# Optimization experiments

Measured on AMD Instinct MI355X. Metric: run time of the kernel, lower is better.

## Reference

```python
import jax, jax.numpy as jnp
import numpy as np

DIM = 1024
N_HEAD = 16
HEAD_DIM = DIM // N_HEAD


def setup_inputs() -> dict:
    key = jax.random.key(0)
    ks = jax.random.split(key, 5)
    scale = 0.02
    x = jax.random.normal(ks[0], (4, 2048, DIM), dtype=jnp.float32)
    W_qkv = jax.random.normal(ks[1], (DIM, 3 * DIM), dtype=jnp.float32) * scale
    b_qkv = jnp.zeros((3 * DIM,), dtype=jnp.float32)
    W_proj = jax.random.normal(ks[2], (DIM, DIM), dtype=jnp.float32) * scale
    b_proj = jnp.zeros((DIM,), dtype=jnp.float32)
    return {"x": x, "W_qkv": W_qkv, "b_qkv": b_qkv, "W_proj": W_proj, "b_proj": b_proj}


def reference(x, W_qkv, b_qkv, W_proj, b_proj):
    B, N, C = x.shape
    qkv = x @ W_qkv + b_qkv                       # [B,N,3C]
    qkv = qkv.reshape(B, N, 3, N_HEAD, HEAD_DIM)
    q, k, v = qkv[:, :, 0], qkv[:, :, 1], qkv[:, :, 2]   # [B,N,H,d]
    # scores: [B,H,N,N]
    att = jnp.einsum('bnhd,bmhd->bhnm', q, k) * (1.0 / np.sqrt(HEAD_DIM))
    att = jax.nn.softmax(att, axis=-1)
    out = jnp.einsum('bhnm,bmhd->bnhd', att, v).reshape(B, N, C)
    return out @ W_proj + b_proj
```

## Files before the change

### kernel.cpp

```cpp
#include <hip/hip_runtime.h>
#include <stdint.h>

#define DEV __device__ __forceinline__

typedef __bf16 bf16x8 __attribute__((ext_vector_type(8)));
typedef float f32x2 __attribute__((ext_vector_type(2)));
typedef float f32x4 __attribute__((ext_vector_type(4)));
typedef float f32x16 __attribute__((ext_vector_type(16)));

DEV uint16_t f2bf(float f) {
  union { float f; uint32_t u; } v; v.f = f;
  return (uint16_t)((v.u + 0x7FFFu + ((v.u >> 16) & 1u)) >> 16);
}

DEV f32x2 pkadd(f32x2 a, f32x2 b) {
  f32x2 d;
  asm("v_pk_add_f32 %0, %1, %2" : "=v"(d) : "v"(a), "v"(b));
  return d;
}

#define GLD_LDS(gsrc, ldst)                                                   \
  __builtin_amdgcn_global_load_lds(                                           \
      (__attribute__((address_space(1))) void*)(void*)(gsrc),                 \
      (__attribute__((address_space(3))) void*)(ldst), 16, 0, 0)

__global__ __launch_bounds__(256) void k_prep(const float* __restrict__ x,
                                              const float* __restrict__ Wqkv,
                                              const float* __restrict__ Wproj,
                                              uint16_t* __restrict__ xb,
                                              uint16_t* __restrict__ wqkvt,
                                              uint16_t* __restrict__ wprojt) {
  __shared__ float tile[32][33];
  int bid = blockIdx.x;
  if (bid < 4096) {
    int i = bid * 256 + threadIdx.x;
    const float4* p = (const float4*)x;
    float4 a = p[i * 2], b = p[i * 2 + 1];
    union { uint16_t s[8]; uint4 v; } o;
    o.s[0] = f2bf(a.x); o.s[1] = f2bf(a.y); o.s[2] = f2bf(a.z); o.s[3] = f2bf(a.w);
    o.s[4] = f2bf(b.x); o.s[5] = f2bf(b.y); o.s[6] = f2bf(b.z); o.s[7] = f2bf(b.w);
    ((uint4*)xb)[i] = o.v;
    return;
  }
  const float* in;
  uint16_t* out;
  int n0, k0, Ncols;
  if (bid < 7168) {
    int local = bid - 4096;
    in = Wqkv; out = wqkvt; Ncols = 3072;
    n0 = (local % 96) * 32; k0 = (local / 96) * 32;
  } else {
    int local = bid - 7168;
    in = Wproj; out = wprojt; Ncols = 1024;
    n0 = (local % 32) * 32; k0 = (local / 32) * 32;
  }
  int tx = threadIdx.x & 31, ty = threadIdx.x >> 5;
  #pragma unroll
  for (int r = ty; r < 32; r += 8)
    tile[r][tx] = in[(size_t)(k0 + r) * Ncols + n0 + tx];
  __syncthreads();
  #pragma unroll
  for (int r = ty; r < 32; r += 8)
    out[(size_t)(n0 + r) * 1024 + k0 + tx] = f2bf(tile[tx][r]);
}

template <int MODE>
__global__ __launch_bounds__(256) void k_gemm(
    const uint16_t* __restrict__ A, const uint16_t* __restrict__ BT,
    const float* __restrict__ bias, float* __restrict__ fout, int Ndim,
    uint16_t* __restrict__ qb, uint16_t* __restrict__ kb,
    uint16_t* __restrict__ vtb) {
  __shared__ uint16_t As[2][128 * 32];
  __shared__ uint16_t Bs[2][128 * 32];
  const int K = 1024;
  int tid = threadIdx.x;
  int lane = tid & 63, wid = tid >> 6;
  int lg = lane >> 4, lr = lane & 15;
  int wr = wid >> 1, wc = wid & 1;
  int bm = blockIdx.x, bn = blockIdx.y;

  int c0 = tid, c1 = tid + 256;
  int r0 = c0 >> 2, sl0 = (c0 & 3) ^ (r0 & 3);
  int r1 = c1 >> 2, sl1 = (c1 & 3) ^ (r1 & 3);
  const uint16_t* gA0 = A + (size_t)(bm * 128 + r0) * K + sl0 * 8;
  const uint16_t* gA1 = A + (size_t)(bm * 128 + r1) * K + sl1 * 8;
  const uint16_t* gB0 = BT + (size_t)(bn * 128 + r0) * K + sl0 * 8;
  const uint16_t* gB1 = BT + (size_t)(bn * 128 + r1) * K + sl1 * 8;

  uint32_t aoff[4], boff[4];
  #pragma unroll
  for (int i = 0; i < 4; ++i) {
    int rowa = wr * 64 + i * 16 + lr;
    aoff[i] = rowa * 64 + ((lg ^ (rowa & 3)) << 4);
    int rowb = wc * 64 + i * 16 + lr;
    boff[i] = rowb * 64 + ((lg ^ (rowb & 3)) << 4);
  }

  f32x4 acc[4][4] = {};

  auto stageg = [&](int buf) {
    GLD_LDS(gA0, &As[buf][wid * 512]);
    GLD_LDS(gA1, &As[buf][2048 + wid * 512]);
    GLD_LDS(gB0, &Bs[buf][wid * 512]);
    GLD_LDS(gB1, &Bs[buf][2048 + wid * 512]);
    gA0 += 32; gA1 += 32; gB0 += 32; gB1 += 32;
  };

  auto gbody = [&](int cur, bool dostage) {
    if (dostage) stageg(cur ^ 1);
    const char* Ab = (const char*)As + cur * 8192;
    const char* Bb = (const char*)Bs + cur * 8192;
    bf16x8 af[4], bfv[4];
    #pragma unroll
    for (int i = 0; i < 4; ++i) af[i] = *(const bf16x8*)(Ab + aoff[i]);
    #pragma unroll
    for (int j = 0; j < 4; ++j) bfv[j] = *(const bf16x8*)(Bb + boff[j]);
    __builtin_amdgcn_s_setprio(1);
    #pragma unroll
    for (int i = 0; i < 4; ++i)
      #pragma unroll
      for (int j = 0; j < 4; ++j)
        acc[i][j] = __builtin_amdgcn_mfma_f32_16x16x32_bf16(af[i], bfv[j],
                                                            acc[i][j], 0, 0, 0);
    __builtin_amdgcn_s_setprio(0);
    __syncthreads();
  };

  stageg(0);
  __syncthreads();
  for (int ks = 0; ks < 30; ks += 2) {
    gbody(0, true);
    gbody(1, true);
  }
  gbody(0, true);
  gbody(1, false);

  int m0 = bm * 128 + wr * 64;
  int n0 = bn * 128 + wc * 64;
  if (MODE == 1) {
    #pragma unroll
    for (int i = 0; i < 4; ++i) {
      int row = m0 + i * 16 + lg * 4;
      #pragma unroll
      for (int j = 0; j < 4; ++j) {
        int col = n0 + j * 16 + lr;
        float bv = bias[col];
        #pragma unroll
        for (int r = 0; r < 4; ++r)
          fout[(size_t)(row + r) * Ndim + col] = acc[i][j][r] + bv;
      }
    }
  } else {
    const float QSC = 0.18033688011112042f;
    #pragma unroll
    for (int i = 0; i < 4; ++i) {
      int rowb = m0 + i * 16 + lg * 4;
      int b = rowb >> 11, t = rowb & 2047;
      #pragma unroll
      for (int j = 0; j < 4; ++j) {
        int colb = n0 + j * 16 + lr;
        int which = colb >> 10;
        int hd = colb & 1023;
        int h = hd >> 6, d = hd & 63;
        float bv = bias[colb];
        size_t bh = (size_t)(b * 16 + h);
        if (which == 2) {
          union { uint16_t s[4]; uint2 v; } pk;
          #pragma unroll
          for (int r = 0; r < 4; ++r) pk.s[r] = f2bf(acc[i][j][r] + bv);
          *(uint2*)&vtb[(bh * 64 + d) * 2048 + t] = pk.v;
        } else {
          uint16_t* dst = which ? kb : qb;
          float sc = which ? 1.f : QSC;
          #pragma unroll
          for (int r = 0; r < 4; ++r)
            dst[(bh * 2048 + t + r) * 64 + d] = f2bf((acc[i][j][r] + bv) * sc);
        }
      }
    }
  }
}

__global__ __launch_bounds__(256) void k_attn(const uint16_t* __restrict__ qb,
                                              const uint16_t* __restrict__ kb,
                                              const uint16_t* __restrict__ vtb,
                                              uint16_t* __restrict__ ob) {
  __shared__ uint16_t SM[4][64 * 64];
  int tid = threadIdx.x, lane = tid & 63, wid = tid >> 6;
  int l31 = lane & 31, hi = lane >> 5;
  int rx = (l31 & 7) ^ (((l31 >> 3) & 3) << 1);
  int bid = blockIdx.x;
  int bh = (bid & 7) * 8 + ((bid >> 3) & 7);
  int qt = bid >> 6;
  const uint16_t* qbh = qb + (size_t)bh * 2048 * 64;
  const uint16_t* kbh = kb + (size_t)bh * 2048 * 64;
  const uint16_t* vbh = vtb + (size_t)bh * 64 * 2048;
  int q = qt * 128 + wid * 32 + l31;

  uint32_t koff[8];
  #pragma unroll
  for (int kvt = 0; kvt < 2; ++kvt)
    #pragma unroll
    for (int ks = 0; ks < 4; ++ks)
      koff[kvt * 4 + ks] = (kvt * 32 + l31) * 128 + (((ks * 2 + hi) ^ rx) << 4);

  bf16x8 qf[4];
  #pragma unroll
  for (int ks = 0; ks < 4; ++ks)
    qf[ks] = *(const bf16x8*)(qbh + (size_t)q * 64 + ks * 16 + hi * 8);

  f32x16 ovt[2] = {};
  f32x2 lr2 = {0.f, 0.f};

  int r0 = tid >> 3;
  int sx = (tid & 7) ^ (r0 & 7) ^ (((r0 >> 3) & 3) << 1);
  const uint16_t* kp0 = kbh + (size_t)r0 * 64 + sx * 8;
  const uint16_t* kp1 = kbh + (size_t)(r0 + 32) * 64 + sx * 8;
  const uint16_t* vp0 = vbh + (size_t)r0 * 2048 + sx * 8;
  const uint16_t* vp1 = vbh + (size_t)(r0 + 32) * 2048 + sx * 8;

  auto stage = [&](int buf) {
    uint16_t* KN = &SM[buf][0];
    uint16_t* VN = &SM[2 + buf][0];
    GLD_LDS(kp0, KN + wid * 512);
    GLD_LDS(kp1, KN + 2048 + wid * 512);
    GLD_LDS(vp0, VN + wid * 512);
    GLD_LDS(vp1, VN + 2048 + wid * 512);
    kp0 += 4096; kp1 += 4096; vp0 += 64; vp1 += 64;
  };

  auto body = [&](int cur, bool dostage) {
    if (dostage) stage(cur ^ 1);
    const char* Kc = (const char*)SM + cur * 8192;
    const char* Vc = (const char*)SM + 16384 + cur * 8192;

    f32x16 sv[2] = {};
    __builtin_amdgcn_s_setprio(1);
    #pragma unroll
    for (int kvt = 0; kvt < 2; ++kvt)
      #pragma unroll
      for (int ks = 0; ks < 4; ++ks) {
        bf16x8 kf = *(const bf16x8*)(Kc + koff[kvt * 4 + ks]);
        sv[kvt] = __builtin_amdgcn_mfma_f32_32x32x16_bf16(kf, qf[ks], sv[kvt], 0, 0, 0);
      }
    __builtin_amdgcn_s_setprio(0);

    #pragma unroll
    for (int t = 0; t < 2; ++t)
      #pragma unroll
      for (int r = 0; r < 16; ++r) sv[t][r] = __builtin_amdgcn_exp2f(sv[t][r]);

    #define SVP(t, i) __builtin_shufflevector(sv[t], sv[t], 2 * (i), 2 * (i) + 1)
    f32x2 s0 = pkadd(pkadd(pkadd(SVP(0, 0), SVP(0, 1)), pkadd(SVP(0, 2), SVP(0, 3))),
                     pkadd(pkadd(SVP(0, 4), SVP(0, 5)), pkadd(SVP(0, 6), SVP(0, 7))));
    f32x2 s1 = pkadd(pkadd(pkadd(SVP(1, 0), SVP(1, 1)), pkadd(SVP(1, 2), SVP(1, 3))),
                     pkadd(pkadd(SVP(1, 4), SVP(1, 5)), pkadd(SVP(1, 6), SVP(1, 7))));
    #undef SVP
    lr2 = pkadd(lr2, pkadd(s0, s1));

    union PB { uint32_t w[4]; bf16x8 v; } pb[4];
    #pragma unroll
    for (int t = 0; t < 2; ++t)
      #pragma unroll
      for (int s = 0; s < 2; ++s) {
        int rb = s * 8;
        #pragma unroll
        for (int i = 0; i < 2; ++i) {
          uint32_t a, b;
          asm("v_cvt_pk_bf16_f32 %0, %1, %2"
              : "=v"(a) : "v"(sv[t][rb + 2 * i]), "v"(sv[t][rb + 2 * i + 1]));
          asm("v_cvt_pk_bf16_f32 %0, %1, %2"
              : "=v"(b) : "v"(sv[t][rb + 4 + 2 * i]), "v"(sv[t][rb + 4 + 2 * i + 1]));
          asm("v_permlane32_swap_b32 %0, %1" : "+v"(a), "+v"(b));
          pb[2 * t + s].w[i] = a;
          pb[2 * t + s].w[2 + i] = b;
        }
      }

    __builtin_amdgcn_s_setprio(1);
    #pragma unroll
    for (int dt = 0; dt < 2; ++dt)
      #pragma unroll
      for (int ks = 0; ks < 4; ++ks) {
        bf16x8 vf = *(const bf16x8*)(Vc + koff[dt * 4 + ks]);
        ovt[dt] = __builtin_amdgcn_mfma_f32_32x32x16_bf16(vf, pb[ks].v, ovt[dt], 0, 0, 0);
      }
    __builtin_amdgcn_s_setprio(0);

    __syncthreads();
  };

  stage(0);
  __syncthreads();
  for (int t = 0; t < 30; t += 2) {
    body(0, true);
    body(1, true);
  }
  body(0, true);
  body(1, false);

  float lrow = lr2.x + lr2.y;
  lrow += __shfl_xor(lrow, 32);
  float inv = 1.f / lrow;
  int b = bh >> 4, h = bh & 15;
  size_t base = ((size_t)b * 2048 + q) * 1024 + h * 64;
  #pragma unroll
  for (int dt = 0; dt < 2; ++dt)
    #pragma unroll
    for (int r = 0; r < 16; r += 2) {
      int d = dt * 32 + (r & 3) + 8 * (r >> 2) + 4 * hi;
      uint32_t w = (uint32_t)f2bf(ovt[dt][r] * inv) |
                   ((uint32_t)f2bf(ovt[dt][r + 1] * inv) << 16);
      *(uint32_t*)&ob[base + d] = w;
    }
}

extern "C" void kernel_launch(void* const* d_in, const int* in_sizes, int n_in,
                              void* d_out, int out_size, void* d_ws,
                              size_t ws_size, hipStream_t stream) {
  const float* x = (const float*)d_in[0];
  const float* Wqkv = (const float*)d_in[1];
  const float* bqkv = (const float*)d_in[2];
  const float* Wproj = (const float*)d_in[3];
  const float* bproj = (const float*)d_in[4];
  float* out = (float*)d_out;
  char* ws = (char*)d_ws;

  uint16_t* xb = (uint16_t*)(ws);
  uint16_t* wqkvt = (uint16_t*)(ws + (16ull << 20));
  uint16_t* wprojt = (uint16_t*)(ws + (22ull << 20));
  uint16_t* qbuf = (uint16_t*)(ws + (24ull << 20));
  uint16_t* kbuf = (uint16_t*)(ws + (40ull << 20));
  uint16_t* vtb = (uint16_t*)(ws + (56ull << 20));
  uint16_t* ob = xb;

  k_prep<<<8192, 256, 0, stream>>>(x, Wqkv, Wproj, xb, wqkvt, wprojt);
  k_gemm<0><<<dim3(64, 24), 256, 0, stream>>>(xb, wqkvt, bqkv, nullptr, 3072,
                                              qbuf, kbuf, vtb);
  k_attn<<<1024, 256, 0, stream>>>(qbuf, kbuf, vtb, ob);
  k_gemm<1><<<dim3(64, 8), 256, 0, stream>>>(ob, wprojt, bproj, out, 1024,
                                             nullptr, nullptr, nullptr);
}
```

Before: 200.5 us.

## Pre-tile V in MFMA fragment order and load it directly to registers

```diff
diff --git a/kernel.cpp b/kernel.cpp
--- a/kernel.cpp
+++ b/kernel.cpp
@@ -168,7 +168,10 @@
           union { uint16_t s[4]; uint2 v; } pk;
           #pragma unroll
           for (int r = 0; r < 4; ++r) pk.s[r] = f2bf(acc[i][j][r] + bv);
-          *(uint2*)&vtb[(bh * 64 + d) * 2048 + t] = pk.v;
+          size_t vidx = bh * 131072 + (size_t)(t >> 6) * 4096 +
+                        (size_t)((d >> 5) * 4 + ((t >> 4) & 3)) * 512 +
+                        (size_t)((((t >> 3) & 1) * 32 + (d & 31)) * 8) + (t & 7);
+          *(uint2*)&vtb[vidx] = pk.v;
         } else {
           uint16_t* dst = which ? kb : qb;
           float sc = which ? 1.f : QSC;
@@ -185,7 +188,7 @@
                                               const uint16_t* __restrict__ kb,
                                               const uint16_t* __restrict__ vtb,
                                               uint16_t* __restrict__ ob) {
-  __shared__ uint16_t SM[4][64 * 64];
+  __shared__ uint16_t Ks[2][64 * 64];
   int tid = threadIdx.x, lane = tid & 63, wid = tid >> 6;
   int l31 = lane & 31, hi = lane >> 5;
   int rx = (l31 & 7) ^ (((l31 >> 3) & 3) << 1);
@@ -194,7 +197,6 @@
   int qt = bid >> 6;
   const uint16_t* qbh = qb + (size_t)bh * 2048 * 64;
   const uint16_t* kbh = kb + (size_t)bh * 2048 * 64;
-  const uint16_t* vbh = vtb + (size_t)bh * 64 * 2048;
   int q = qt * 128 + wid * 32 + l31;
 
   uint32_t koff[8];
@@ -216,23 +218,23 @@
   int sx = (tid & 7) ^ (r0 & 7) ^ (((r0 >> 3) & 3) << 1);
   const uint16_t* kp0 = kbh + (size_t)r0 * 64 + sx * 8;
   const uint16_t* kp1 = kbh + (size_t)(r0 + 32) * 64 + sx * 8;
-  const uint16_t* vp0 = vbh + (size_t)r0 * 2048 + sx * 8;
-  const uint16_t* vp1 = vbh + (size_t)(r0 + 32) * 2048 + sx * 8;
+  const uint16_t* vp = vtb + (size_t)bh * 131072 + (size_t)lane * 8;
 
   auto stage = [&](int buf) {
-    uint16_t* KN = &SM[buf][0];
-    uint16_t* VN = &SM[2 + buf][0];
+    uint16_t* KN = &Ks[buf][0];
     GLD_LDS(kp0, KN + wid * 512);
     GLD_LDS(kp1, KN + 2048 + wid * 512);
-    GLD_LDS(vp0, VN + wid * 512);
-    GLD_LDS(vp1, VN + 2048 + wid * 512);
-    kp0 += 4096; kp1 += 4096; vp0 += 64; vp1 += 64;
+    kp0 += 4096; kp1 += 4096;
   };
 
   auto body = [&](int cur, bool dostage) {
+    bf16x8 vf[8];
+    #pragma unroll
+    for (int f = 0; f < 8; ++f) vf[f] = *(const bf16x8*)(vp + f * 512);
+    vp += 4096;
+
     if (dostage) stage(cur ^ 1);
-    const char* Kc = (const char*)SM + cur * 8192;
-    const char* Vc = (const char*)SM + 16384 + cur * 8192;
+    const char* Kc = (const char*)Ks + cur * 8192;
 
     f32x16 sv[2] = {};
     __builtin_amdgcn_s_setprio(1);
@@ -281,10 +283,9 @@
     #pragma unroll
     for (int dt = 0; dt < 2; ++dt)
       #pragma unroll
-      for (int ks = 0; ks < 4; ++ks) {
-        bf16x8 vf = *(const bf16x8*)(Vc + koff[dt * 4 + ks]);
-        ovt[dt] = __builtin_amdgcn_mfma_f32_32x32x16_bf16(vf, pb[ks].v, ovt[dt], 0, 0, 0);
-      }
+      for (int ks = 0; ks < 4; ++ks)
+        ovt[dt] = __builtin_amdgcn_mfma_f32_32x32x16_bf16(vf[dt * 4 + ks], pb[ks].v,
+                                                          ovt[dt], 0, 0, 0);
     __builtin_amdgcn_s_setprio(0);
 
     __syncthreads();
```

Measured after the change: 199.1 us. About the same (-0.7%).
